# Kernel optimization log

Measured on AMD Instinct MI355X. Metric: run time of the kernel, lower is better.

Reference implementation:

```python
import jax, jax.numpy as jnp
import numpy as np
from jax import lax

BN_EPS = 1e-5
DIST_EPS = 1e-8

def _three_nn_interpolate(xyz1, xyz2, points2):
    # squared pairwise distances: (B, N, S)
    d2 = (jnp.sum(xyz1 ** 2, -1)[:, :, None]
          + jnp.sum(xyz2 ** 2, -1)[:, None, :]
          - 2.0 * jnp.einsum('bnd,bsd->bns', xyz1, xyz2))
    neg_d, idx = lax.top_k(-d2, 3)            # 3 nearest -> (B, N, 3)
    dist = -neg_d
    recip = 1.0 / (dist + DIST_EPS)
    weight = recip / jnp.sum(recip, -1, keepdims=True)   # (B, N, 3)
    gathered = jax.vmap(lambda p, i: p[i])(points2, idx)  # (B, N, 3, C2)
    return jnp.einsum('bnkc,bnk->bnc', gathered, weight)

def _conv_bn_relu(x, w, g, b):
    # x: (B, N, Cin); 1x1 conv == matmul; BatchNorm1d over (B, N) per channel (training stats)
    y = jnp.einsum('bnc,oc->bno', x, w)
    mu = jnp.mean(y, axis=(0, 1))
    var = jnp.mean((y - mu) ** 2, axis=(0, 1))
    yn = (y - mu) * lax.rsqrt(var + BN_EPS)
    return jax.nn.relu(yn * g + b)

def setup_inputs() -> dict:
    key = jax.random.key(0)
    ks = jax.random.split(key, 6)
    B, N, S, C1, C2 = 16, 4096, 1024, 256, 256
    return {
        'xyz1': jax.random.normal(ks[0], (B, N, 3), jnp.float32),
        'xyz2': jax.random.normal(ks[1], (B, S, 3), jnp.float32),
        'points1': jax.random.normal(ks[2], (B, N, C1), jnp.float32),
        'points2': jax.random.normal(ks[3], (B, S, C2), jnp.float32),
        'w1': jax.random.normal(ks[4], (256, C1 + C2), jnp.float32) * 0.04,
        'g1': jnp.ones((256,), jnp.float32),
        'b1': jnp.zeros((256,), jnp.float32),
        'w2': jax.random.normal(ks[5], (256, 256), jnp.float32) * 0.06,
        'g2': jnp.ones((256,), jnp.float32),
        'b2': jnp.zeros((256,), jnp.float32),
    }

def reference(xyz1, xyz2, points1, points2, w1, g1, b1, w2, g2, b2):
    interp = _three_nn_interpolate(xyz1, xyz2, points2)    # (B, N, C2)
    feats = jnp.concatenate([points1, interp], axis=-1)    # (B, N, C1+C2)
    h = _conv_bn_relu(feats, w1, g1, b1)
    out = _conv_bn_relu(h, w2, g2, b2)
    return out                                              # (B, N, 256)
```

## Files before the change

kernel.cpp:

```cpp
#include <hip/hip_runtime.h>
#include <stdint.h>

typedef unsigned short ushort_t;
typedef __bf16 bf16x8 __attribute__((ext_vector_type(8)));
typedef float f32x4 __attribute__((ext_vector_type(4)));
typedef unsigned short ushort8 __attribute__((ext_vector_type(8)));
typedef unsigned short ushort4_t __attribute__((ext_vector_type(4)));

#define DEV static __device__ __forceinline__

DEV unsigned short f2bf(float f) {
    union { float f; unsigned int i; } v; v.f = f;
    unsigned int u = v.i;
    return (unsigned short)((u + 0x7fffu + ((u >> 16) & 1u)) >> 16);
}
DEV float bf2f(unsigned short u) {
    union { unsigned int i; float f; } v; v.i = ((unsigned int)u) << 16; return v.f;
}
DEV bf16x8 u2b(ushort8 u) { union { ushort8 u; bf16x8 b; } x; x.u = u; return x.b; }

__global__ __launch_bounds__(256) void cvt_kernel(
    const float* __restrict__ in, ushort_t* __restrict__ out, int n)
{
    int i = blockIdx.x * 256 + threadIdx.x;
    if (i < n) out[i] = f2bf(in[i]);
}

__global__ __launch_bounds__(256) void cvt4_kernel(
    const float* __restrict__ in, ushort_t* __restrict__ out)
{
    int i = (blockIdx.x * 256 + threadIdx.x) * 4;
    float4 v = *(const float4*)(in + i);
    ushort4_t o;
    o[0] = f2bf(v.x); o[1] = f2bf(v.y); o[2] = f2bf(v.z); o[3] = f2bf(v.w);
    *(ushort4_t*)(out + i) = o;
}

__global__ __launch_bounds__(256) void knn_kernel(
    const float* __restrict__ xyz1, const float* __restrict__ xyz2,
    int* __restrict__ idx_out, float* __restrict__ w_out)
{
    __shared__ float4 P[1024];
    __shared__ float mD[24][32];
    __shared__ int   mI[24][32];
    const int b = blockIdx.y;
    const int tid = threadIdx.x;
    for (int s = tid; s < 1024; s += 256) {
        const float* p = xyz2 + ((size_t)b * 1024 + s) * 3;
        float x = p[0], y = p[1], z = p[2];
        float pp = __fadd_rn(__fadd_rn(__fmul_rn(x, x), __fmul_rn(y, y)), __fmul_rn(z, z));
        P[s] = make_float4(x, y, z, pp);
    }
    __syncthreads();
    const int ql = tid & 31;
    const int chunk = tid >> 5;
    const int n = blockIdx.x * 32 + ql;
    const float* q = xyz1 + ((size_t)b * 4096 + n) * 3;
    float qx = q[0], qy = q[1], qz = q[2];
    float qq = __fadd_rn(__fadd_rn(__fmul_rn(qx, qx), __fmul_rn(qy, qy)), __fmul_rn(qz, qz));
    float d0 = 1e30f, d1 = 1e30f, d2 = 1e30f;
    int i0 = 0, i1 = 0, i2 = 0;
    const int s0 = chunk * 128;
#pragma unroll 4
    for (int s = s0; s < s0 + 128; ++s) {
        float4 p = P[s];
        float dot = __fadd_rn(__fadd_rn(__fmul_rn(qx, p.x), __fmul_rn(qy, p.y)), __fmul_rn(qz, p.z));
        float d = __fsub_rn(__fadd_rn(qq, p.w), __fmul_rn(2.0f, dot));
        if (d < d2) {
            if (d < d1) {
                d2 = d1; i2 = i1;
                if (d < d0) { d1 = d0; i1 = i0; d0 = d; i0 = s; }
                else        { d1 = d;  i1 = s; }
            } else { d2 = d; i2 = s; }
        }
    }
    mD[chunk * 3 + 0][ql] = d0; mI[chunk * 3 + 0][ql] = i0;
    mD[chunk * 3 + 1][ql] = d1; mI[chunk * 3 + 1][ql] = i1;
    mD[chunk * 3 + 2][ql] = d2; mI[chunk * 3 + 2][ql] = i2;
    __syncthreads();
    if (tid < 32) {
        float e0 = 1e30f, e1 = 1e30f, e2 = 1e30f;
        int j0 = 0, j1 = 0, j2 = 0;
#pragma unroll
        for (int c = 0; c < 24; ++c) {
            float d = mD[c][ql]; int i = mI[c][ql];
            if (d < e2) {
                if (d < e1) {
                    e2 = e1; j2 = j1;
                    if (d < e0) { e1 = e0; j1 = j0; e0 = d; j0 = i; }
                    else        { e1 = d;  j1 = i; }
                } else { e2 = d; j2 = i; }
            }
        }
        float r0 = 1.0f / (e0 + 1e-8f);
        float r1 = 1.0f / (e1 + 1e-8f);
        float r2 = 1.0f / (e2 + 1e-8f);
        float rs = __fadd_rn(__fadd_rn(r0, r1), r2);
        size_t o = ((size_t)b * 4096 + n) * 3;
        idx_out[o + 0] = j0; idx_out[o + 1] = j1; idx_out[o + 2] = j2;
        w_out[o + 0] = r0 / rs; w_out[o + 1] = r1 / rs; w_out[o + 2] = r2 / rs;
    }
}

__global__ __launch_bounds__(256) void interp_kernel(
    const ushort_t* __restrict__ p2b, const int* __restrict__ idx,
    const float* __restrict__ wgt, ushort_t* __restrict__ itp)
{
    const int t = blockIdx.x * 256 + threadIdx.x;
    const int q = t >> 3;
    const int cg = (t & 7) * 32;
    const size_t o = (size_t)q * 3;
    int i0 = idx[o], i1 = idx[o + 1], i2 = idx[o + 2];
    float w0 = wgt[o], w1 = wgt[o + 1], w2 = wgt[o + 2];
    const ushort_t* pb = p2b + (size_t)(q >> 12) * (1024 * 256);
    const ushort8* g0 = (const ushort8*)(pb + (size_t)i0 * 256 + cg);
    const ushort8* g1 = (const ushort8*)(pb + (size_t)i1 * 256 + cg);
    const ushort8* g2 = (const ushort8*)(pb + (size_t)i2 * 256 + cg);
    ushort8* dst = (ushort8*)(itp + (size_t)q * 256 + cg);
#pragma unroll
    for (int s = 0; s < 4; ++s) {
        ushort8 a = g0[s], b = g1[s], c = g2[s];
        ushort8 ov;
#pragma unroll
        for (int j = 0; j < 8; ++j) {
            float acc = __fmul_rn(w0, bf2f(a[j]));
            acc = fmaf(w1, bf2f(b[j]), acc);
            acc = fmaf(w2, bf2f(c[j]), acc);
            ov[j] = f2bf(acc);
        }
        dst[s] = ov;
    }
}

DEV void cvt8(const float4& u0, const float4& u1, ushort8& hv) {
    hv[0] = f2bf(u0.x); hv[1] = f2bf(u0.y); hv[2] = f2bf(u0.z); hv[3] = f2bf(u0.w);
    hv[4] = f2bf(u1.x); hv[5] = f2bf(u1.y); hv[6] = f2bf(u1.z); hv[7] = f2bf(u1.w);
}

__global__ __launch_bounds__(512, 4) void gemm1_kernel(
    const float* __restrict__ p1, const ushort_t* __restrict__ itp,
    const ushort_t* __restrict__ w1b, ushort_t* __restrict__ y,
    float* __restrict__ sums, float* __restrict__ sqs)
{
    __shared__ __align__(16) char smem[66560];
    ushort_t* Bs = (ushort_t*)smem;
    const int tid = threadIdx.x;
    const int wave = tid >> 6, lane = tid & 63;
    const int frl = lane & 15, fq = lane >> 4;
    const int panel = blockIdx.x >> 2, nb = blockIdx.x & 3;
    const int m0 = panel * 256;

    {
        const int c = tid >> 3, qq = tid & 7;
        const ushort_t* src = w1b + (size_t)(nb * 64 + c) * 512;
        ushort_t* dst = Bs + c * 520;
#pragma unroll
        for (int s = 0; s < 8; ++s) {
            int off = qq * 8 + s * 64;
            *(ushort8*)(dst + off) = *(const ushort8*)(src + off);
        }
    }

    f32x4 acc[2][4];
#pragma unroll
    for (int i = 0; i < 2; ++i)
#pragma unroll
        for (int j = 0; j < 4; ++j) acc[i][j] = f32x4{0.0f, 0.0f, 0.0f, 0.0f};

    __syncthreads();

    const int row0 = m0 + wave * 32 + frl;
    bf16x8 afb[2][2], bfb[2][4];

#define G1_LOADA(buf, kc) {                                                        \
    if ((kc) < 8) {                                                                \
        _Pragma("unroll")                                                          \
        for (int i = 0; i < 2; ++i) {                                              \
            const float4* g = (const float4*)(p1 + (size_t)(row0 + i * 16) * 256   \
                                              + (kc) * 32 + fq * 8);               \
            float4 u0 = g[0], u1 = g[1];                                           \
            ushort8 hv; cvt8(u0, u1, hv);                                          \
            buf[i] = u2b(hv);                                                      \
        }                                                                          \
    } else {                                                                       \
        _Pragma("unroll")                                                          \
        for (int i = 0; i < 2; ++i)                                                \
            buf[i] = *(const bf16x8*)(itp + (size_t)(row0 + i * 16) * 256          \
                                      + ((kc) - 8) * 32 + fq * 8);                 \
    } }
#define G1_LOADB(buf, kc) { _Pragma("unroll")                                      \
    for (int j = 0; j < 4; ++j)                                                    \
        buf[j] = *(const bf16x8*)(Bs + (j * 16 + frl) * 520 + (kc) * 32 + fq * 8); }

    G1_LOADA(afb[0], 0); G1_LOADB(bfb[0], 0);
#pragma unroll
    for (int kc = 0; kc < 16; ++kc) {
        const int cur = kc & 1, nxt = cur ^ 1;
        if (kc < 15) { G1_LOADA(afb[nxt], kc + 1); G1_LOADB(bfb[nxt], kc + 1); }
#pragma unroll
        for (int i = 0; i < 2; ++i)
#pragma unroll
            for (int j = 0; j < 4; ++j)
                acc[i][j] = __builtin_amdgcn_mfma_f32_16x16x32_bf16(afb[cur][i], bfb[cur][j], acc[i][j], 0, 0, 0);
    }

    float ps[4], pq[4];
#pragma unroll
    for (int j = 0; j < 4; ++j) {
        const int colg = nb * 64 + j * 16 + frl;
        float s = 0.f, q = 0.f;
#pragma unroll
        for (int i = 0; i < 2; ++i)
#pragma unroll
            for (int rr = 0; rr < 4; ++rr) {
                ushort_t hb = f2bf(acc[i][j][rr]);
                float v = bf2f(hb);
                y[(size_t)(m0 + wave * 32 + i * 16 + fq * 4 + rr) * 256 + colg] = hb;
                s += v; q = fmaf(v, v, q);
            }
        s += __shfl_xor(s, 16); s += __shfl_xor(s, 32);
        q += __shfl_xor(q, 16); q += __shfl_xor(q, 32);
        ps[j] = s; pq[j] = q;
    }
    __syncthreads();
    float* scrS = (float*)smem;
    float* scrQ = (float*)(smem + 2048);
    if (fq == 0) {
#pragma unroll
        for (int j = 0; j < 4; ++j) {
            scrS[wave * 64 + j * 16 + frl] = ps[j];
            scrQ[wave * 64 + j * 16 + frl] = pq[j];
        }
    }
    __syncthreads();
    if (tid < 64) {
        float s = 0.f, q = 0.f;
#pragma unroll
        for (int w = 0; w < 8; ++w) { s += scrS[w * 64 + tid]; q += scrQ[w * 64 + tid]; }
        atomicAdd(&sums[nb * 64 + tid], s);
        atomicAdd(&sqs[nb * 64 + tid], q);
    }
}

__global__ __launch_bounds__(512, 2) void gemm2_kernel(
    const ushort_t* __restrict__ y1, const ushort_t* __restrict__ w2b,
    const float* __restrict__ a1, const float* __restrict__ c1,
    ushort_t* __restrict__ y2, float* __restrict__ sums, float* __restrict__ sqs)
{
    __shared__ __align__(16) char smem[137216];
    ushort_t* As = (ushort_t*)smem;
    ushort_t* Bs = (ushort_t*)(smem + 67584);
    float* sAv = (float*)(smem + 135168);
    float* sCv = (float*)(smem + 136192);
    const int tid = threadIdx.x;
    const int wave = tid >> 6, lane = tid & 63;
    const int frl = lane & 15, fq = lane >> 4;
    const int panel = blockIdx.x >> 1, nb = blockIdx.x & 1;
    const int m0 = panel * 128;

    if (tid < 256) { sAv[tid] = a1[tid]; sCv[tid] = c1[tid]; }
    __syncthreads();

    {
        const int r = tid >> 2, qq = tid & 3;
        const ushort_t* srcA = y1 + (size_t)(m0 + r) * 256;
        ushort_t* dstA = As + r * 264;
        const ushort_t* srcB = w2b + (size_t)(nb * 128 + r) * 256;
        ushort_t* dstB = Bs + r * 264;
#pragma unroll
        for (int s = 0; s < 8; ++s) {
            int off = qq * 8 + s * 32;
            ushort8 raw = *(const ushort8*)(srcA + off);
            ushort8 hv;
#pragma unroll
            for (int e = 0; e < 8; ++e) {
                float v = bf2f(raw[e]);
                hv[e] = f2bf(fmaxf(fmaf(v, sAv[off + e], sCv[off + e]), 0.0f));
            }
            *(ushort8*)(dstA + off) = hv;
            *(ushort8*)(dstB + off) = *(const ushort8*)(srcB + off);
        }
    }

    f32x4 acc[2][4];
#pragma unroll
    for (int i = 0; i < 2; ++i)
#pragma unroll
        for (int j = 0; j < 4; ++j) acc[i][j] = f32x4{0.0f, 0.0f, 0.0f, 0.0f};

    __syncthreads();

    const int rg = (wave & 3) * 32, cg = (wave >> 2) * 64;
    bf16x8 afb[2][2], bfb[2][4];

#define G2_LOADA(buf, kc) { _Pragma("unroll")                                      \
    for (int i = 0; i < 2; ++i)                                                    \
        buf[i] = *(const bf16x8*)(As + (rg + i * 16 + frl) * 264 + (kc) * 32 + fq * 8); }
#define G2_LOADB(buf, kc) { _Pragma("unroll")                                      \
    for (int j = 0; j < 4; ++j)                                                    \
        buf[j] = *(const bf16x8*)(Bs + (cg + j * 16 + frl) * 264 + (kc) * 32 + fq * 8); }

    G2_LOADA(afb[0], 0); G2_LOADB(bfb[0], 0);
#pragma unroll
    for (int kc = 0; kc < 8; ++kc) {
        const int cur = kc & 1, nxt = cur ^ 1;
        if (kc < 7) { G2_LOADA(afb[nxt], kc + 1); G2_LOADB(bfb[nxt], kc + 1); }
#pragma unroll
        for (int i = 0; i < 2; ++i)
#pragma unroll
            for (int j = 0; j < 4; ++j)
                acc[i][j] = __builtin_amdgcn_mfma_f32_16x16x32_bf16(afb[cur][i], bfb[cur][j], acc[i][j], 0, 0, 0);
    }

    float ps[4], pq[4];
#pragma unroll
    for (int j = 0; j < 4; ++j) {
        const int colg = nb * 128 + cg + j * 16 + frl;
        float s = 0.f, q = 0.f;
#pragma unroll
        for (int i = 0; i < 2; ++i)
#pragma unroll
            for (int rr = 0; rr < 4; ++rr) {
                ushort_t hb = f2bf(acc[i][j][rr]);
                float v = bf2f(hb);
                y2[(size_t)(m0 + rg + i * 16 + fq * 4 + rr) * 256 + colg] = hb;
                s += v; q = fmaf(v, v, q);
            }
        s += __shfl_xor(s, 16); s += __shfl_xor(s, 32);
        q += __shfl_xor(q, 16); q += __shfl_xor(q, 32);
        ps[j] = s; pq[j] = q;
    }
    __syncthreads();
    float* scrS = (float*)smem;
    float* scrQ = (float*)(smem + 2048);
    if (fq == 0) {
#pragma unroll
        for (int j = 0; j < 4; ++j) {
            scrS[wave * 64 + j * 16 + frl] = ps[j];
            scrQ[wave * 64 + j * 16 + frl] = pq[j];
        }
    }
    __syncthreads();
    if (tid < 128) {
        const int g = tid >> 6, cw = tid & 63;
        float s = 0.f, q = 0.f;
#pragma unroll
        for (int k = 0; k < 4; ++k) {
            s += scrS[(g * 4 + k) * 64 + cw];
            q += scrQ[(g * 4 + k) * 64 + cw];
        }
        atomicAdd(&sums[nb * 128 + g * 64 + cw], s);
        atomicAdd(&sqs[nb * 128 + g * 64 + cw], q);
    }
}

__global__ __launch_bounds__(256) void finalize_kernel(
    const float* __restrict__ sums, const float* __restrict__ sqs,
    const float* __restrict__ g, const float* __restrict__ bias,
    float* __restrict__ a, float* __restrict__ c)
{
    const int ch = threadIdx.x;
    const float inv_n = 1.0f / 65536.0f;
    float mu = sums[ch] * inv_n;
    float var = fmaf(-mu, mu, sqs[ch] * inv_n);
    float is = 1.0f / sqrtf(var + 1e-5f);
    float aa = g[ch] * is;
    a[ch] = aa;
    c[ch] = fmaf(-mu, aa, bias[ch]);
}

__global__ __launch_bounds__(256) void apply_kernel(
    const ushort_t* __restrict__ y2, const float* __restrict__ a,
    const float* __restrict__ c, float* __restrict__ out)
{
    const size_t i = ((size_t)blockIdx.x * 256 + threadIdx.x) * 8;
    const int ch = (int)(i & 255);
    ushort8 raw = *(const ushort8*)(y2 + i);
    float4 o0, o1;
    const float4 a0 = *(const float4*)(a + ch), a1v = *(const float4*)(a + ch + 4);
    const float4 c0 = *(const float4*)(c + ch), c1v = *(const float4*)(c + ch + 4);
    o0.x = fmaxf(fmaf(bf2f(raw[0]), a0.x, c0.x), 0.0f);
    o0.y = fmaxf(fmaf(bf2f(raw[1]), a0.y, c0.y), 0.0f);
    o0.z = fmaxf(fmaf(bf2f(raw[2]), a0.z, c0.z), 0.0f);
    o0.w = fmaxf(fmaf(bf2f(raw[3]), a0.w, c0.w), 0.0f);
    o1.x = fmaxf(fmaf(bf2f(raw[4]), a1v.x, c1v.x), 0.0f);
    o1.y = fmaxf(fmaf(bf2f(raw[5]), a1v.y, c1v.y), 0.0f);
    o1.z = fmaxf(fmaf(bf2f(raw[6]), a1v.z, c1v.z), 0.0f);
    o1.w = fmaxf(fmaf(bf2f(raw[7]), a1v.w, c1v.w), 0.0f);
    *(float4*)(out + i) = o0;
    *(float4*)(out + i + 4) = o1;
}

extern "C" void kernel_launch(void* const* d_in, const int* in_sizes, int n_in,
                              void* d_out, int out_size, void* d_ws, size_t ws_size,
                              hipStream_t stream)
{
    const float* xyz1    = (const float*)d_in[0];
    const float* xyz2    = (const float*)d_in[1];
    const float* points1 = (const float*)d_in[2];
    const float* points2 = (const float*)d_in[3];
    const float* w1      = (const float*)d_in[4];
    const float* g1      = (const float*)d_in[5];
    const float* b1      = (const float*)d_in[6];
    const float* w2      = (const float*)d_in[7];
    const float* g2      = (const float*)d_in[8];
    const float* b2      = (const float*)d_in[9];
    float* out = (float*)d_out;

    char* ws = (char*)d_ws;
    float* sums1 = (float*)(ws + 0);
    float* sqs1  = (float*)(ws + 1024);
    float* a1    = (float*)(ws + 2048);
    float* c1    = (float*)(ws + 3072);
    float* sums2 = (float*)(ws + 4096);
    float* sqs2  = (float*)(ws + 5120);
    float* a2    = (float*)(ws + 6144);
    float* c2    = (float*)(ws + 7168);
    ushort_t* w1b = (ushort_t*)(ws + (64u << 10));
    ushort_t* w2b = (ushort_t*)(ws + (320u << 10));
    ushort_t* p2b = (ushort_t*)(ws + (1u << 20));
    int*   idx   = (int*)(ws + (10u << 20));
    float* wgt   = (float*)(ws + (11u << 20));
    ushort_t* itp = (ushort_t*)(ws + (12u << 20));
    ushort_t* y1  = (ushort_t*)(ws + (44u << 20));
    ushort_t* y2b = itp;

    hipMemsetAsync(ws, 0, 8192, stream);
    cvt_kernel<<<dim3(512), 256, 0, stream>>>(w1, w1b, 131072);
    cvt_kernel<<<dim3(256), 256, 0, stream>>>(w2, w2b, 65536);
    cvt4_kernel<<<dim3(4096), 256, 0, stream>>>(points2, p2b);
    knn_kernel<<<dim3(128, 16), 256, 0, stream>>>(xyz1, xyz2, idx, wgt);
    interp_kernel<<<dim3(2048), 256, 0, stream>>>(p2b, idx, wgt, itp);
    gemm1_kernel<<<dim3(1024), 512, 0, stream>>>(points1, itp, w1b, y1, sums1, sqs1);
    finalize_kernel<<<dim3(1), 256, 0, stream>>>(sums1, sqs1, g1, b1, a1, c1);
    gemm2_kernel<<<dim3(1024), 512, 0, stream>>>(y1, w2b, a1, c1, y2b, sums2, sqs2);
    finalize_kernel<<<dim3(1), 256, 0, stream>>>(sums2, sqs2, g2, b2, a2, c2);
    apply_kernel<<<dim3(8192), 256, 0, stream>>>(y2b, a2, c2, out);
}
```

Before: 320.7 us.

## Retile gemm1 to 256x128 blocks with double-buffered LDS staging of A and B

Result: faster. 296.1 us (-7.7%).

```diff
diff --git a/kernel.cpp b/kernel.cpp
--- a/kernel.cpp
+++ b/kernel.cpp
@@ -142,89 +142,103 @@
     const ushort_t* __restrict__ w1b, ushort_t* __restrict__ y,
     float* __restrict__ sums, float* __restrict__ sqs)
 {
-    __shared__ __align__(16) char smem[66560];
-    ushort_t* Bs = (ushort_t*)smem;
+    __shared__ __align__(16) ushort_t smem[30720];
+    ushort_t* const Ab0 = smem;
+    ushort_t* const Bb0 = smem + 10240;
+    ushort_t* const Ab1 = smem + 15360;
+    ushort_t* const Bb1 = smem + 25600;
     const int tid = threadIdx.x;
     const int wave = tid >> 6, lane = tid & 63;
     const int frl = lane & 15, fq = lane >> 4;
-    const int panel = blockIdx.x >> 2, nb = blockIdx.x & 3;
+    const int wr = wave & 3, wc = wave >> 2;
+    const int panel = blockIdx.x >> 1, nb = blockIdx.x & 1;
     const int m0 = panel * 256;
-
-    {
-        const int c = tid >> 3, qq = tid & 7;
-        const ushort_t* src = w1b + (size_t)(nb * 64 + c) * 512;
-        ushort_t* dst = Bs + c * 520;
-#pragma unroll
-        for (int s = 0; s < 8; ++s) {
-            int off = qq * 8 + s * 64;
-            *(ushort8*)(dst + off) = *(const ushort8*)(src + off);
-        }
-    }
-
-    f32x4 acc[2][4];
-#pragma unroll
-    for (int i = 0; i < 2; ++i)
+    const int ar = tid >> 1, akk = (tid & 1) * 16;
+    const int bc = tid >> 2, bkk = (tid & 3) * 8;
+
+    float4 la0, la1, la2, la3;
+    ushort8 lab0, lab1;
+    ushort8 lb;
+
+#define G1_LOADT(t) {                                                              \
+    if ((t) < 8) {                                                                 \
+        const float4* g = (const float4*)(p1 + (size_t)(m0 + ar) * 256             \
+                                          + (t) * 32 + akk);                       \
+        la0 = g[0]; la1 = g[1]; la2 = g[2]; la3 = g[3];                            \
+    } else {                                                                       \
+        const ushort8* g = (const ushort8*)(itp + (size_t)(m0 + ar) * 256          \
+                                            + ((t) - 8) * 32 + akk);               \
+        lab0 = g[0]; lab1 = g[1];                                                  \
+    }                                                                              \
+    lb = *(const ushort8*)(w1b + (size_t)(nb * 128 + bc) * 512 + (t) * 32 + bkk); }
+
+#define G1_WRITET(t, Abuf, Bbuf) {                                                 \
+    ushort_t* ad = (Abuf) + ar * 40 + akk;                                         \
+    if ((t) < 8) {                                                                 \
+        ushort8 h0, h1; cvt8(la0, la1, h0); cvt8(la2, la3, h1);                    \
+        *(ushort8*)ad = h0; *(ushort8*)(ad + 8) = h1;                              \
+    } else {                                                                       \
+        *(ushort8*)ad = lab0; *(ushort8*)(ad + 8) = lab1;                          \
+    }                                                                              \
+    *(ushort8*)((Bbuf) + bc * 40 + bkk) = lb; }
+
+#define G1_STEP(Abuf, Bbuf) {                                                      \
+    bf16x8 af[4], bf[4];                                                           \
+    _Pragma("unroll")                                                              \
+    for (int i = 0; i < 4; ++i)                                                    \
+        af[i] = *(const bf16x8*)((Abuf) + (wr * 64 + i * 16 + frl) * 40 + fq * 8); \
+    _Pragma("unroll")                                                              \
+    for (int j = 0; j < 4; ++j)                                                    \
+        bf[j] = *(const bf16x8*)((Bbuf) + (wc * 64 + j * 16 + frl) * 40 + fq * 8); \
+    _Pragma("unroll")                                                              \
+    for (int i = 0; i < 4; ++i)                                                    \
+        _Pragma("unroll")                                                          \
+        for (int j = 0; j < 4; ++j)                                                \
+            acc[i][j] = __builtin_amdgcn_mfma_f32_16x16x32_bf16(af[i], bf[j], acc[i][j], 0, 0, 0); }
+
+    f32x4 acc[4][4];
+#pragma unroll
+    for (int i = 0; i < 4; ++i)
 #pragma unroll
         for (int j = 0; j < 4; ++j) acc[i][j] = f32x4{0.0f, 0.0f, 0.0f, 0.0f};
 
-    __syncthreads();
-
-    const int row0 = m0 + wave * 32 + frl;
-    bf16x8 afb[2][2], bfb[2][4];
-
-#define G1_LOADA(buf, kc) {                                                        \
-    if ((kc) < 8) {                                                                \
-        _Pragma("unroll")                                                          \
-        for (int i = 0; i < 2; ++i) {                                              \
-            const float4* g = (const float4*)(p1 + (size_t)(row0 + i * 16) * 256   \
-                                              + (kc) * 32 + fq * 8);               \
-            float4 u0 = g[0], u1 = g[1];                                           \
-            ushort8 hv; cvt8(u0, u1, hv);                                          \
-            buf[i] = u2b(hv);                                                      \
-        }                                                                          \
-    } else {                                                                       \
-        _Pragma("unroll")                                                          \
-        for (int i = 0; i < 2; ++i)                                                \
-            buf[i] = *(const bf16x8*)(itp + (size_t)(row0 + i * 16) * 256          \
-                                      + ((kc) - 8) * 32 + fq * 8);                 \
-    } }
-#define G1_LOADB(buf, kc) { _Pragma("unroll")                                      \
-    for (int j = 0; j < 4; ++j)                                                    \
-        buf[j] = *(const bf16x8*)(Bs + (j * 16 + frl) * 520 + (kc) * 32 + fq * 8); }
-
-    G1_LOADA(afb[0], 0); G1_LOADB(bfb[0], 0);
-#pragma unroll
-    for (int kc = 0; kc < 16; ++kc) {
-        const int cur = kc & 1, nxt = cur ^ 1;
-        if (kc < 15) { G1_LOADA(afb[nxt], kc + 1); G1_LOADB(bfb[nxt], kc + 1); }
-#pragma unroll
-        for (int i = 0; i < 2; ++i)
-#pragma unroll
-            for (int j = 0; j < 4; ++j)
-                acc[i][j] = __builtin_amdgcn_mfma_f32_16x16x32_bf16(afb[cur][i], bfb[cur][j], acc[i][j], 0, 0, 0);
+    G1_LOADT(0);
+    G1_WRITET(0, Ab0, Bb0);
+    __syncthreads();
+
+#pragma unroll
+    for (int t = 0; t < 16; ++t) {
+        if (t < 15) G1_LOADT(t + 1);
+        if ((t & 1) == 0) {
+            G1_STEP(Ab0, Bb0);
+            if (t < 15) G1_WRITET(t + 1, Ab1, Bb1);
+        } else {
+            G1_STEP(Ab1, Bb1);
+            if (t < 15) G1_WRITET(t + 1, Ab0, Bb0);
+        }
+        __syncthreads();
     }
 
     float ps[4], pq[4];
 #pragma unroll
     for (int j = 0; j < 4; ++j) {
-        const int colg = nb * 64 + j * 16 + frl;
+        const int colg = nb * 128 + wc * 64 + j * 16 + frl;
         float s = 0.f, q = 0.f;
 #pragma unroll
-        for (int i = 0; i < 2; ++i)
+        for (int i = 0; i < 4; ++i)
 #pragma unroll
             for (int rr = 0; rr < 4; ++rr) {
                 ushort_t hb = f2bf(acc[i][j][rr]);
                 float v = bf2f(hb);
-                y[(size_t)(m0 + wave * 32 + i * 16 + fq * 4 + rr) * 256 + colg] = hb;
+                y[(size_t)(m0 + wr * 64 + i * 16 + fq * 4 + rr) * 256 + colg] = hb;
                 s += v; q = fmaf(v, v, q);
             }
         s += __shfl_xor(s, 16); s += __shfl_xor(s, 32);
         q += __shfl_xor(q, 16); q += __shfl_xor(q, 32);
         ps[j] = s; pq[j] = q;
     }
-    __syncthreads();
     float* scrS = (float*)smem;
-    float* scrQ = (float*)(smem + 2048);
+    float* scrQ = (float*)(smem + 4096);
     if (fq == 0) {
 #pragma unroll
         for (int j = 0; j < 4; ++j) {
@@ -233,12 +247,16 @@
         }
     }
     __syncthreads();
-    if (tid < 64) {
+    if (tid < 128) {
+        const int g = tid >> 6, cw = tid & 63;
         float s = 0.f, q = 0.f;
 #pragma unroll
-        for (int w = 0; w < 8; ++w) { s += scrS[w * 64 + tid]; q += scrQ[w * 64 + tid]; }
-        atomicAdd(&sums[nb * 64 + tid], s);
-        atomicAdd(&sqs[nb * 64 + tid], q);
+        for (int k = 0; k < 4; ++k) {
+            s += scrS[(g * 4 + k) * 64 + cw];
+            q += scrQ[(g * 4 + k) * 64 + cw];
+        }
+        atomicAdd(&sums[nb * 128 + g * 64 + cw], s);
+        atomicAdd(&sqs[nb * 128 + g * 64 + cw], q);
     }
 }
 
@@ -431,7 +449,7 @@
     cvt4_kernel<<<dim3(4096), 256, 0, stream>>>(points2, p2b);
     knn_kernel<<<dim3(128, 16), 256, 0, stream>>>(xyz1, xyz2, idx, wgt);
     interp_kernel<<<dim3(2048), 256, 0, stream>>>(p2b, idx, wgt, itp);
-    gemm1_kernel<<<dim3(1024), 512, 0, stream>>>(points1, itp, w1b, y1, sums1, sqs1);
+    gemm1_kernel<<<dim3(512), 512, 0, stream>>>(points1, itp, w1b, y1, sums1, sqs1);
     finalize_kernel<<<dim3(1), 256, 0, stream>>>(sums1, sqs1, g1, b1, a1, c1);
     gemm2_kernel<<<dim3(1024), 512, 0, stream>>>(y1, w2b, a1, c1, y2b, sums2, sqs2);
     finalize_kernel<<<dim3(1), 256, 0, stream>>>(sums2, sqs2, g2, b2, a2, c2);
```
